# Kernel tuning notes

Measured on AMD Instinct MI355X. Metric: run time of the kernel, lower is better.

## Reference

```python
import jax, jax.numpy as jnp
import numpy as np

B, A, C, M, E = 8, 100000, 8, 128, 32
ALPHA, GAMMA = 0.25, 2.0


def setup_inputs() -> dict:
    key = jax.random.key(0)
    k1, k2, k3, k4, k5, k6, k7 = jax.random.split(key, 7)
    classifications = jax.random.uniform(k1, (B, A, C), dtype=jnp.float32)
    regressions = jax.random.normal(k2, (B, A, 8), dtype=jnp.float32)
    embeddings = jax.random.normal(k3, (B, A, E), dtype=jnp.float32)
    # anchors: random centers on a 1920x1080 image, reasonable w/h -> x1,y1,x2,y2
    cx = jax.random.uniform(k4, (A,), minval=0.0, maxval=1920.0)
    cy = jax.random.uniform(jax.random.fold_in(k4, 1), (A,), minval=0.0, maxval=1080.0)
    w = jax.random.uniform(jax.random.fold_in(k4, 2), (A,), minval=16.0, maxval=256.0)
    h = jax.random.uniform(jax.random.fold_in(k4, 3), (A,), minval=16.0, maxval=256.0)
    anchors = jnp.stack([cx - 0.5 * w, cy - 0.5 * h, cx + 0.5 * w, cy + 0.5 * h], axis=1)[None].astype(jnp.float32)
    # annotations: 16 coords = jittered 3D-box corner projections around a random box,
    # col 16 = object id, col 17 = class label in [0, C)
    bcx = jax.random.uniform(k5, (B, M, 1), minval=100.0, maxval=1820.0)
    bcy = jax.random.uniform(jax.random.fold_in(k5, 1), (B, M, 1), minval=100.0, maxval=980.0)
    bw = jax.random.uniform(jax.random.fold_in(k5, 2), (B, M, 1), minval=30.0, maxval=300.0)
    bh = jax.random.uniform(jax.random.fold_in(k5, 3), (B, M, 1), minval=30.0, maxval=300.0)
    jit = jax.random.uniform(k6, (B, M, 16), minval=-0.4, maxval=0.4)
    sx = jnp.array([-1, -1, 1, 1, -1, -1, 1, 1], jnp.float32)
    sy = jnp.array([-1, 1, -1, 1, -1, 1, -1, 1], jnp.float32)
    xs = bcx + 0.5 * bw * (sx + jit[..., 0:16:2])
    ys = bcy + 0.5 * bh * (sy + jit[..., 1:16:2])
    coords = jnp.stack([xs, ys], axis=-1).reshape(B, M, 16)
    ids = jax.random.randint(k7, (B, M, 1), 0, 1000).astype(jnp.float32)
    cls_lab = jax.random.randint(jax.random.fold_in(k7, 1), (B, M, 1), 0, C).astype(jnp.float32)
    annotations = jnp.concatenate([coords, ids, cls_lab], axis=-1)
    return {
        "classifications": classifications,
        "regressions": regressions,
        "anchors": anchors,
        "annotations": annotations,
        "embeddings": embeddings,
    }


def calc_iou(a, b):
    # a: [A,4], b: [M,4] in x1,y1,x2,y2 -> [A,M]
    area = (b[:, 2] - b[:, 0]) * (b[:, 3] - b[:, 1])
    iw = jnp.minimum(a[:, 2:3], b[None, :, 2]) - jnp.maximum(a[:, 0:1], b[None, :, 0])
    ih = jnp.minimum(a[:, 3:4], b[None, :, 3]) - jnp.maximum(a[:, 1:2], b[None, :, 1])
    iw = jnp.clip(iw, 0.0)
    ih = jnp.clip(ih, 0.0)
    ua = ((a[:, 2] - a[:, 0]) * (a[:, 3] - a[:, 1]))[:, None] + area[None, :] - iw * ih
    return iw * ih / jnp.clip(ua, 1e-8)


_S2 = jnp.array([-1, -1, 1, 1, -1, -1, 1, 1], jnp.float32)
_S4 = jnp.array([-1, 1, -1, 1, -1, 1, -1, 1], jnp.float32)
_S6 = jnp.array([1, 1, 1, 1, -1, -1, -1, -1], jnp.float32)


def _per_image(cls, reg, ann, anchor):
    # cls [A,C], reg [A,8], ann [M,18], anchor [A,4]
    aw = anchor[:, 2] - anchor[:, 0]
    ah = anchor[:, 3] - anchor[:, 1]
    acx = anchor[:, 0] + 0.5 * aw
    acy = anchor[:, 1] + 0.5 * ah
    cls = jnp.clip(cls, 1e-4, 1.0 - 1e-4)
    valid = ann[:, -1] >= 0.0  # [M]; annotations with class -1 are padding
    xs, ys = ann[:, 0:16:2], ann[:, 1:16:2]
    box2d = jnp.stack([xs.min(1), ys.min(1), xs.max(1), ys.max(1)], axis=1)  # [M,4]
    iou = jnp.where(valid[None, :], calc_iou(anchor, box2d), -1.0)  # [A,M]
    iou_max = iou.max(1)
    assigned = ann[iou.argmax(1)]  # [A,18]
    pos = iou_max >= 0.5
    neg = iou_max < 0.4
    num_pos = jnp.maximum(pos.sum().astype(cls.dtype), 1.0)

    onehot = jax.nn.one_hot(assigned[:, -1].astype(jnp.int32), cls.shape[1], dtype=cls.dtype)
    targets = jnp.where(pos[:, None], onehot, jnp.where(neg[:, None], 0.0, -1.0))
    alpha_f = jnp.where(targets == 1.0, ALPHA, 1.0 - ALPHA)
    focal_w = alpha_f * jnp.where(targets == 1.0, 1.0 - cls, cls) ** GAMMA
    bce = -(targets * jnp.log(cls) + (1.0 - targets) * jnp.log(1.0 - cls))
    cls_loss = jnp.where(targets != -1.0, focal_w * bce, 0.0).sum() / num_pos

    t = assigned[:, :16]

    def vp(rx, ry, tx, ty):
        denom = jnp.sqrt(rx * rx + ry * ry) * jnp.sqrt(tx * tx + ty * ty)
        return 1.0 - (rx * tx + ry * ty) / jnp.maximum(denom, 1e-8)

    vp1 = vp(reg[:, 2], reg[:, 3],
             (t[:, 4] + t[:, 6] + t[:, 12] + t[:, 14] - (t[:, 0] + t[:, 2] + t[:, 8] + t[:, 10])) / 4.0,
             (t[:, 5] + t[:, 7] + t[:, 13] + t[:, 15] - (t[:, 1] + t[:, 3] + t[:, 9] + t[:, 11])) / 4.0)
    vp2 = vp(reg[:, 4], reg[:, 5],
             (t[:, 2] + t[:, 6] + t[:, 10] + t[:, 14] - (t[:, 0] + t[:, 4] + t[:, 8] + t[:, 12])) / 4.0,
             (t[:, 3] + t[:, 7] + t[:, 11] + t[:, 15] - (t[:, 1] + t[:, 5] + t[:, 9] + t[:, 13])) / 4.0)
    vp3 = vp(reg[:, 6], reg[:, 7],
             (t[:, 0] + t[:, 2] + t[:, 4] + t[:, 6] - (t[:, 8] + t[:, 10] + t[:, 12] + t[:, 14])) / 4.0,
             (t[:, 1] + t[:, 3] + t[:, 5] + t[:, 7] - (t[:, 9] + t[:, 11] + t[:, 13] + t[:, 15])) / 4.0)
    vp_all = (vp1 + vp2 + vp3) / 3.0
    vp_loss = (vp_all * pos).sum() / num_pos

    # corner predictions from (ctr_x, ctr_y, v1, v2, v3) offsets: [A,8] x-coords, [A,8] y-coords
    px = reg[:, 0:1] + reg[:, 2:3] * _S2 + reg[:, 4:5] * _S4 + reg[:, 6:7] * _S6
    py = reg[:, 1:2] + reg[:, 3:4] * _S2 + reg[:, 5:6] * _S4 + reg[:, 7:8] * _S6
    tx = (t[:, 0:16:2] - acx[:, None]) / aw[:, None]
    ty = (t[:, 1:16:2] - acy[:, None]) / ah[:, None]
    diff = jnp.concatenate([jnp.abs(px - tx), jnp.abs(py - ty)], axis=1)  # [A,16]
    sl1 = jnp.where(diff <= 1.0 / 9.0, 0.5 * 9.0 * diff * diff, diff - 0.5 / 9.0)
    reg_loss = (sl1.mean(1) * pos).sum() / num_pos
    return cls_loss, reg_loss, vp_loss


def reference(classifications, regressions, anchors, annotations, embeddings):
    anchor = anchors[0]
    cls_l, reg_l, vp_l = jax.vmap(_per_image, in_axes=(0, 0, 0, None))(
        classifications, regressions, annotations, anchor)
    return jnp.stack([cls_l.mean(), reg_l.mean(), vp_l.mean()])


if __name__ == "__main__":
    print(reference(**setup_inputs()))
```

## Files before the change

kernel.cpp:

```cpp
#include <hip/hip_runtime.h>

namespace {

constexpr int B_N = 8;
constexpr int A_N = 100000;
constexpr int M_N = 128;
constexpr int BLOCK = 256;
constexpr int NBLK_S = (A_N + BLOCK - 1) / BLOCK;
constexpr int GX = 16, GY = 9, NC = GX * GY;
constexpr float CELL = 120.0f;
constexpr float MARGIN = 128.0f;
constexpr int CPC = 4;
constexpr int NCH = NC * CPC;

constexpr size_t OFF_HIST = 0;
constexpr size_t OFF_OFFS = OFF_HIST + (size_t)NBLK_S * NC * 4;
constexpr size_t OFF_CT   = OFF_OFFS + (size_t)NC * NBLK_S * 4;
constexpr size_t OFF_CB   = OFF_CT + NC * 4;
constexpr size_t OFF_SIDX = (OFF_CB + (NC + 1) * 4 + 15) & ~size_t(15);
constexpr size_t OFF_SANC = (OFF_SIDX + (size_t)A_N * 4 + 15) & ~size_t(15);
constexpr size_t OFF_SNEG = OFF_SANC + (size_t)A_N * 16;
constexpr size_t OFF_PART = OFF_SNEG + (size_t)B_N * A_N * 4;

__device__ __forceinline__ int cell_of(const float4& an) {
    const float acx = 0.5f * (an.x + an.z);
    const float acy = 0.5f * (an.y + an.w);
    const int cx = min(GX - 1, max(0, (int)(acx * (1.0f / CELL))));
    const int cy = min(GY - 1, max(0, (int)(acy * (1.0f / CELL))));
    return cy * GX + cx;
}

__global__ __launch_bounds__(BLOCK) void s1k(
    const float* __restrict__ anchors_,
    const float* __restrict__ cls_,
    unsigned* __restrict__ hist,
    float* __restrict__ sneg_)
{
    __shared__ unsigned h[NC];
    const int tid = threadIdx.x, blk = blockIdx.x;
    for (int i = tid; i < NC; i += BLOCK) h[i] = 0u;
    __syncthreads();
    const int a = blk * BLOCK + tid;
    if (a < A_N) {
        const float4 an = ((const float4*)anchors_)[a];
        atomicAdd(&h[cell_of(an)], 1u);
#pragma unroll
        for (int b = 0; b < B_N; ++b) {
            const float* cp = cls_ + ((size_t)b * A_N + a) * 8;
            const float4 cA = ((const float4*)cp)[0];
            const float4 cB = ((const float4*)cp)[1];
            const float pv[8] = {cA.x, cA.y, cA.z, cA.w, cB.x, cB.y, cB.z, cB.w};
            float s = 0.f;
#pragma unroll
            for (int c = 0; c < 8; ++c) {
                const float p = fminf(fmaxf(pv[c], 1e-4f), 1.0f - 1e-4f);
                s += 0.75f * p * p * (-__logf(1.0f - p));
            }
            sneg_[(size_t)b * A_N + a] = s;
        }
    }
    __syncthreads();
    for (int i = tid; i < NC; i += BLOCK) hist[(size_t)blk * NC + i] = h[i];
}

__global__ __launch_bounds__(BLOCK) void s2a_scan(
    const unsigned* __restrict__ hist,
    unsigned* __restrict__ offs,
    unsigned* __restrict__ cellTot)
{
    const int c = blockIdx.x, t = threadIdx.x;
    const int k0 = 2 * t, k1 = 2 * t + 1;
    const unsigned v0 = (k0 < NBLK_S) ? hist[(size_t)k0 * NC + c] : 0u;
    const unsigned v1 = (k1 < NBLK_S) ? hist[(size_t)k1 * NC + c] : 0u;
    const unsigned mysum = v0 + v1;
    __shared__ unsigned s[BLOCK];
    s[t] = mysum;
    __syncthreads();
    for (int off = 1; off < BLOCK; off <<= 1) {
        const unsigned x = (t >= off) ? s[t - off] : 0u;
        __syncthreads();
        s[t] += x;
        __syncthreads();
    }
    const unsigned excl = s[t] - mysum;
    if (k0 < NBLK_S) offs[(size_t)c * NBLK_S + k0] = excl;
    if (k1 < NBLK_S) offs[(size_t)c * NBLK_S + k1] = excl + v0;
    if (t == BLOCK - 1) cellTot[c] = s[BLOCK - 1];
}

__global__ __launch_bounds__(BLOCK) void s3_scatter(
    const float* __restrict__ anchors_,
    const unsigned* __restrict__ offs,
    const unsigned* __restrict__ cellTot,
    unsigned* __restrict__ cellBase,
    unsigned* __restrict__ sidx, float4* __restrict__ sanc)
{
    __shared__ unsigned sscan[BLOCK];
    __shared__ unsigned scb[NC];
    __shared__ unsigned hw[4][NC];
    const int tid = threadIdx.x, blk = blockIdx.x;

    const unsigned v = (tid < NC) ? cellTot[tid] : 0u;
    sscan[tid] = v;
    for (int i = tid; i < 4 * NC; i += BLOCK) (&hw[0][0])[i] = 0u;
    __syncthreads();
    for (int off = 1; off < BLOCK; off <<= 1) {
        const unsigned x = (tid >= off) ? sscan[tid - off] : 0u;
        __syncthreads();
        sscan[tid] += x;
        __syncthreads();
    }
    if (tid < NC) scb[tid] = sscan[tid] - v;
    if (blk == 0) {
        if (tid < NC) cellBase[tid] = sscan[tid] - v;
        if (tid == NC - 1) cellBase[NC] = sscan[tid];
    }

    const int a = blk * BLOCK + tid;
    const bool valid = (a < A_N);
    float4 an = make_float4(0.f, 0.f, 0.f, 0.f);
    int c = -1;
    if (valid) { an = ((const float4*)anchors_)[a]; c = cell_of(an); }
    const int ln = tid & 63, wv = tid >> 6;

    int rank = 0, cnt = 0;
    for (int j = 0; j < 64; ++j) {
        const int cj = __shfl(c, j);
        const bool same = (cj == c);
        rank += (same && (j < ln));
        cnt  += same;
    }
    if (valid && rank == 0) hw[wv][c] = (unsigned)cnt;
    __syncthreads();
    if (valid) {
        unsigned r = (unsigned)rank;
        for (int w = 0; w < wv; ++w) r += hw[w][c];
        const unsigned d = scb[c] + offs[(size_t)c * NBLK_S + blk] + r;
        sidx[d] = (unsigned)a;
        sanc[d] = an;
    }
}

__global__ __launch_bounds__(BLOCK) void ka2(
    const float* __restrict__ cls_,
    const float* __restrict__ reg_,
    const float* __restrict__ ann_,
    const float* __restrict__ sneg_,
    const unsigned* __restrict__ cellBase,
    const unsigned* __restrict__ sidx,
    const float4* __restrict__ sanc,
    float* __restrict__ partials)
{
    const int cc = blockIdx.x / CPC, chunk = blockIdx.x % CPC;
    const int b = blockIdx.y, tid = threadIdx.x;
    const int base = (int)cellBase[cc];
    const int n    = (int)cellBase[cc + 1] - base;

    if (chunk * BLOCK >= n) {
        if (tid == 0) {
            float* o = partials + ((size_t)b * NCH + blockIdx.x) * 4;
            o[0] = 0.f; o[1] = 0.f; o[2] = 0.f; o[3] = 0.f;
        }
        return;
    }

    __shared__ float s_x1[M_N], s_y1[M_N], s_x2[M_N], s_y2[M_N], s_nb[M_N];
    __shared__ int   s_id[M_N];
    __shared__ unsigned long long s_w[2];
    __shared__ unsigned s_pre[2];
    __shared__ int s_Kv;

    const int ccx = cc % GX, ccy = cc / GX;
    const float lox = ccx * CELL - MARGIN, hix = ccx * CELL + CELL + MARGIN;
    const float loy = ccy * CELL - MARGIN, hiy = ccy * CELL + CELL + MARGIN;
    bool ok = false;
    float minx = 0.f, miny = 0.f, maxx = 0.f, maxy = 0.f, area = 0.f;
    if (tid < M_N) {
        const float* t = ann_ + ((size_t)b * M_N + tid) * 18;
        minx = t[0]; maxx = t[0]; miny = t[1]; maxy = t[1];
#pragma unroll
        for (int j = 1; j < 8; ++j) {
            const float x = t[2 * j], y = t[2 * j + 1];
            minx = fminf(minx, x); maxx = fmaxf(maxx, x);
            miny = fminf(miny, y); maxy = fmaxf(maxy, y);
        }
        area = (maxx - minx) * (maxy - miny);
        ok = (t[17] >= 0.0f) && (minx <= hix) && (maxx >= lox) &&
             (miny <= hiy) && (maxy >= loy);
    }
    const unsigned long long bw = __ballot(ok);
    if (tid < 128 && (tid & 63) == 0) s_w[tid >> 6] = bw;
    __syncthreads();
    if (tid == 0) {
        const unsigned p0 = (unsigned)__popcll(s_w[0]);
        s_pre[0] = 0u; s_pre[1] = p0;
        s_Kv = (int)(p0 + (unsigned)__popcll(s_w[1]));
    }
    __syncthreads();
    if (ok) {
        const int wq = tid >> 6;
        const int r = (int)(s_pre[wq] +
            (unsigned)__popcll(s_w[wq] & ((1ull << (tid & 63)) - 1ull)));
        s_x1[r] = minx; s_y1[r] = miny;
        s_x2[r] = maxx; s_y2[r] = maxy;
        s_nb[r] = -area;
        s_id[r] = tid;
    }
    __syncthreads();
    const int K = s_Kv;

    const int i0  = chunk * BLOCK + tid;
    const bool inb = (i0 < n);
    const int gi  = base + (inb ? i0 : 0);
    const float4 an = sanc[gi];
    const int a = (int)sidx[gi];
    const float sneg_v = sneg_[(size_t)b * A_N + a];

    const float aarea = (an.z - an.x) * (an.w - an.y);
    float m1 = -3e38f, m2 = -3e38f;
    float bn = 0.f, bs = 1.f;
    int   kb = 0;

    for (int m = 0; m < K; ++m) {
        const float x1 = s_x1[m], y1 = s_y1[m];
        const float x2 = s_x2[m], y2 = s_y2[m];
        const float nb = s_nb[m];
        const float iw = fminf(an.z, x2) - fmaxf(an.x, x1);
        const float ih = fminf(an.w, y2) - fmaxf(an.y, y1);
        const float in_ = fmaxf(iw, 0.f) * fmaxf(ih, 0.f);
        m1 = fmaxf(m1, __builtin_fmaf(3.0f, in_, nb));
        m2 = fmaxf(m2, __builtin_fmaf(3.5f, in_, nb));
        const float s = aarea - nb;
        const bool  u = (in_ * bs > bn * s);
        bn = u ? in_ : bn;
        bs = u ? s   : bs;
        kb = u ? m   : kb;
    }

    const bool pos = inb && (m1 >= aarea);
    const bool nonign = pos || (m2 < aarea);

    float clsS = (inb && nonign) ? sneg_v : 0.f;
    float regS = 0.f, vpS = 0.f, posC = 0.f;

    if (pos) {
        posC = 1.0f;
        const float* t = ann_ + ((size_t)b * M_N + s_id[kb]) * 18;
        float tt[16];
#pragma unroll
        for (int j = 0; j < 16; ++j) tt[j] = t[j];
        const int kc = (int)t[17];

        const float praw = cls_[((size_t)b * A_N + a) * 8 + kc];
        const float pkc = fminf(fmaxf(praw, 1e-4f), 1.0f - 1e-4f);
        const float negkc   = 0.75f * pkc * pkc * (-__logf(1.0f - pkc));
        const float posterm = 0.25f * (1.0f - pkc) * (1.0f - pkc) * (-__logf(pkc));
        clsS += posterm - negkc;

        const float aw = an.z - an.x;
        const float ah = an.w - an.y;
        const float* rp = reg_ + ((size_t)b * A_N + a) * 8;
        const float4 r0 = ((const float4*)rp)[0];
        const float4 r1 = ((const float4*)rp)[1];

        auto vp = [](float rx, float ry, float tx, float ty) {
            const float denom = sqrtf(rx * rx + ry * ry) * sqrtf(tx * tx + ty * ty);
            return 1.0f - (rx * tx + ry * ty) / fmaxf(denom, 1e-8f);
        };
        const float vp1 = vp(r0.z, r0.w,
            (tt[4] + tt[6] + tt[12] + tt[14] - (tt[0] + tt[2] + tt[8] + tt[10])) * 0.25f,
            (tt[5] + tt[7] + tt[13] + tt[15] - (tt[1] + tt[3] + tt[9] + tt[11])) * 0.25f);
        const float vp2 = vp(r1.x, r1.y,
            (tt[2] + tt[6] + tt[10] + tt[14] - (tt[0] + tt[4] + tt[8] + tt[12])) * 0.25f,
            (tt[3] + tt[7] + tt[11] + tt[15] - (tt[1] + tt[5] + tt[9] + tt[13])) * 0.25f);
        const float vp3 = vp(r1.z, r1.w,
            (tt[0] + tt[2] + tt[4] + tt[6] - (tt[8] + tt[10] + tt[12] + tt[14])) * 0.25f,
            (tt[1] + tt[3] + tt[5] + tt[7] - (tt[9] + tt[11] + tt[13] + tt[15])) * 0.25f);
        vpS = (vp1 + vp2 + vp3) * (1.0f / 3.0f);

        const float s2v[8] = {-1, -1, 1, 1, -1, -1, 1, 1};
        const float s4v[8] = {-1, 1, -1, 1, -1, 1, -1, 1};
        const float s6v[8] = {1, 1, 1, 1, -1, -1, -1, -1};
        const float acx2 = an.x + 0.5f * aw;
        const float acy2 = an.y + 0.5f * ah;
        float ssum = 0.f;
#pragma unroll
        for (int j = 0; j < 8; ++j) {
            const float px = r0.x + r0.z * s2v[j] + r1.x * s4v[j] + r1.z * s6v[j];
            const float py = r0.y + r0.w * s2v[j] + r1.y * s4v[j] + r1.w * s6v[j];
            const float tx = (tt[2 * j]     - acx2) / aw;
            const float ty = (tt[2 * j + 1] - acy2) / ah;
            const float dx = fabsf(px - tx);
            const float dy = fabsf(py - ty);
            ssum += (dx <= (1.0f / 9.0f)) ? 4.5f * dx * dx : dx - (0.5f / 9.0f);
            ssum += (dy <= (1.0f / 9.0f)) ? 4.5f * dy * dy : dy - (0.5f / 9.0f);
        }
        regS = ssum * (1.0f / 16.0f);
    }

#pragma unroll
    for (int off = 32; off; off >>= 1) {
        clsS += __shfl_down(clsS, off);
        regS += __shfl_down(regS, off);
        vpS  += __shfl_down(vpS, off);
        posC += __shfl_down(posC, off);
    }
    __shared__ float s_red[4][4];
    const int wv = tid >> 6, ln = tid & 63;
    if (ln == 0) {
        s_red[wv][0] = clsS; s_red[wv][1] = regS;
        s_red[wv][2] = vpS;  s_red[wv][3] = posC;
    }
    __syncthreads();
    if (tid == 0) {
        float C = 0, R = 0, V = 0, P = 0;
        for (int w2 = 0; w2 < 4; ++w2) {
            C += s_red[w2][0]; R += s_red[w2][1];
            V += s_red[w2][2]; P += s_red[w2][3];
        }
        float* out = partials + ((size_t)b * NCH + blockIdx.x) * 4;
        out[0] = C; out[1] = R; out[2] = V; out[3] = P;
    }
}

__global__ __launch_bounds__(BLOCK) void kc_final(
    const float* __restrict__ partials,
    float* __restrict__ out)
{
    const int tid = threadIdx.x;
    __shared__ float s[4][4];
    __shared__ float accum[3];
    if (tid == 0) { accum[0] = 0.f; accum[1] = 0.f; accum[2] = 0.f; }

    for (int b = 0; b < B_N; ++b) {
        float c = 0.f, r = 0.f, v = 0.f, p = 0.f;
        for (int i = tid; i < NCH; i += BLOCK) {
            const float* q = partials + ((size_t)b * NCH + i) * 4;
            c += q[0]; r += q[1]; v += q[2]; p += q[3];
        }
#pragma unroll
        for (int off = 32; off; off >>= 1) {
            c += __shfl_down(c, off); r += __shfl_down(r, off);
            v += __shfl_down(v, off); p += __shfl_down(p, off);
        }
        const int wv = tid >> 6, ln = tid & 63;
        if (ln == 0) { s[wv][0] = c; s[wv][1] = r; s[wv][2] = v; s[wv][3] = p; }
        __syncthreads();
        if (tid == 0) {
            float C = 0, R = 0, V = 0, P = 0;
            for (int w = 0; w < 4; ++w) {
                C += s[w][0]; R += s[w][1]; V += s[w][2]; P += s[w][3];
            }
            const float np_ = fmaxf(P, 1.0f);
            accum[0] += C / np_; accum[1] += R / np_; accum[2] += V / np_;
        }
        __syncthreads();
    }
    if (tid == 0) {
        out[0] = accum[0] * 0.125f;
        out[1] = accum[1] * 0.125f;
        out[2] = accum[2] * 0.125f;
    }
}

}

extern "C" void kernel_launch(void* const* d_in, const int* in_sizes, int n_in,
                              void* d_out, int out_size, void* d_ws, size_t ws_size,
                              hipStream_t stream)
{
    const float* cls_    = (const float*)d_in[0];
    const float* reg_    = (const float*)d_in[1];
    const float* anchors = (const float*)d_in[2];
    const float* ann     = (const float*)d_in[3];

    char* ws = (char*)d_ws;
    unsigned* hist     = (unsigned*)(ws + OFF_HIST);
    unsigned* offs     = (unsigned*)(ws + OFF_OFFS);
    unsigned* cellTot  = (unsigned*)(ws + OFF_CT);
    unsigned* cellBase = (unsigned*)(ws + OFF_CB);
    unsigned* sidxp    = (unsigned*)(ws + OFF_SIDX);
    float4*   sancp    = (float4*)(ws + OFF_SANC);
    float*    snegp    = (float*)(ws + OFF_SNEG);
    float*    partials = (float*)(ws + OFF_PART);

    s1k<<<dim3(NBLK_S), dim3(BLOCK), 0, stream>>>(anchors, cls_, hist, snegp);
    s2a_scan<<<dim3(NC), dim3(BLOCK), 0, stream>>>(hist, offs, cellTot);
    s3_scatter<<<dim3(NBLK_S), dim3(BLOCK), 0, stream>>>(anchors, offs, cellTot,
                                                         cellBase, sidxp, sancp);
    ka2<<<dim3(NCH, B_N), dim3(BLOCK), 0, stream>>>(
        cls_, reg_, ann, snegp, cellBase, sidxp, sancp, partials);
    kc_final<<<dim3(1), dim3(BLOCK), 0, stream>>>(partials, (float*)d_out);
}
```

Before: 63.51 us.

## Precompute per-cell box lists and loop batches inside the IoU kernel

Building the per-(batch, cell) filtered annotation lists moves out of the IoU kernel and into the first kernel, which gets extra blocks to write them to a workspace buffer along with counts. The IoU kernel now launches one block per cell chunk instead of one per (chunk, batch). Each block loops over all eight batches, reusing its anchor and index loads and copying the prebuilt box records into shared memory. This removes redundant annotation filtering and anchor reloads, but cuts the grid size eightfold and serializes batch work within a block, which may reduce latency hiding.

```diff
diff --git a/kernel.cpp b/kernel.cpp
--- a/kernel.cpp
+++ b/kernel.cpp
@@ -20,7 +20,9 @@
 constexpr size_t OFF_SIDX = (OFF_CB + (NC + 1) * 4 + 15) & ~size_t(15);
 constexpr size_t OFF_SANC = (OFF_SIDX + (size_t)A_N * 4 + 15) & ~size_t(15);
 constexpr size_t OFF_SNEG = OFF_SANC + (size_t)A_N * 16;
-constexpr size_t OFF_PART = OFF_SNEG + (size_t)B_N * A_N * 4;
+constexpr size_t OFF_BL   = OFF_SNEG + (size_t)B_N * A_N * 4;
+constexpr size_t OFF_KL   = OFF_BL + (size_t)B_N * NC * M_N * 8 * 4;
+constexpr size_t OFF_PART = (OFF_KL + (size_t)B_N * NC * 4 + 15) & ~size_t(15);
 
 __device__ __forceinline__ int cell_of(const float4& an) {
     const float acx = 0.5f * (an.x + an.z);
@@ -30,37 +32,81 @@
     return cy * GX + cx;
 }
 
-__global__ __launch_bounds__(BLOCK) void s1k(
+__global__ __launch_bounds__(BLOCK) void s1kx(
     const float* __restrict__ anchors_,
     const float* __restrict__ cls_,
+    const float* __restrict__ ann_,
     unsigned* __restrict__ hist,
-    float* __restrict__ sneg_)
+    float* __restrict__ sneg_,
+    float* __restrict__ bl,
+    unsigned* __restrict__ kl)
 {
     __shared__ unsigned h[NC];
-    const int tid = threadIdx.x, blk = blockIdx.x;
-    for (int i = tid; i < NC; i += BLOCK) h[i] = 0u;
+    __shared__ unsigned long long s_w[2];
+    __shared__ unsigned s_pre[2];
+    const int blk = blockIdx.x, tid = threadIdx.x;
+
+    if (blk < NBLK_S) {
+        for (int i = tid; i < NC; i += BLOCK) h[i] = 0u;
+        __syncthreads();
+        const int a = blk * BLOCK + tid;
+        if (a < A_N) {
+            const float4 an = ((const float4*)anchors_)[a];
+            atomicAdd(&h[cell_of(an)], 1u);
+#pragma unroll
+            for (int b = 0; b < B_N; ++b) {
+                const float* cp = cls_ + ((size_t)b * A_N + a) * 8;
+                const float4 cA = ((const float4*)cp)[0];
+                const float4 cB = ((const float4*)cp)[1];
+                const float pv[8] = {cA.x, cA.y, cA.z, cA.w, cB.x, cB.y, cB.z, cB.w};
+                float s = 0.f;
+#pragma unroll
+                for (int c = 0; c < 8; ++c) {
+                    const float p = fminf(fmaxf(pv[c], 1e-4f), 1.0f - 1e-4f);
+                    s += 0.75f * p * p * (-__logf(1.0f - p));
+                }
+                sneg_[(size_t)b * A_N + a] = s;
+            }
+        }
+        __syncthreads();
+        for (int i = tid; i < NC; i += BLOCK) hist[(size_t)blk * NC + i] = h[i];
+        return;
+    }
+
+    const int bi = blk - NBLK_S;
+    const int b  = bi / NC, cc = bi % NC;
+    const int ccx = cc % GX, ccy = cc / GX;
+    const float lox = ccx * CELL - MARGIN, hix = ccx * CELL + CELL + MARGIN;
+    const float loy = ccy * CELL - MARGIN, hiy = ccy * CELL + CELL + MARGIN;
+    bool ok = false;
+    float minx = 0.f, miny = 0.f, maxx = 0.f, maxy = 0.f, area = 0.f;
+    if (tid < M_N) {
+        const float* t = ann_ + ((size_t)b * M_N + tid) * 18;
+        minx = t[0]; maxx = t[0]; miny = t[1]; maxy = t[1];
+#pragma unroll
+        for (int j = 1; j < 8; ++j) {
+            const float x = t[2 * j], y = t[2 * j + 1];
+            minx = fminf(minx, x); maxx = fmaxf(maxx, x);
+            miny = fminf(miny, y); maxy = fmaxf(maxy, y);
+        }
+        area = (maxx - minx) * (maxy - miny);
+        ok = (t[17] >= 0.0f) && (minx <= hix) && (maxx >= lox) &&
+             (miny <= hiy) && (maxy >= loy);
+    }
+    const unsigned long long bw = __ballot(ok);
+    if (tid < 128 && (tid & 63) == 0) s_w[tid >> 6] = bw;
     __syncthreads();
-    const int a = blk * BLOCK + tid;
-    if (a < A_N) {
-        const float4 an = ((const float4*)anchors_)[a];
-        atomicAdd(&h[cell_of(an)], 1u);
-#pragma unroll
-        for (int b = 0; b < B_N; ++b) {
-            const float* cp = cls_ + ((size_t)b * A_N + a) * 8;
-            const float4 cA = ((const float4*)cp)[0];
-            const float4 cB = ((const float4*)cp)[1];
-            const float pv[8] = {cA.x, cA.y, cA.z, cA.w, cB.x, cB.y, cB.z, cB.w};
-            float s = 0.f;
-#pragma unroll
-            for (int c = 0; c < 8; ++c) {
-                const float p = fminf(fmaxf(pv[c], 1e-4f), 1.0f - 1e-4f);
-                s += 0.75f * p * p * (-__logf(1.0f - p));
-            }
-            sneg_[(size_t)b * A_N + a] = s;
-        }
-    }
-    __syncthreads();
-    for (int i = tid; i < NC; i += BLOCK) hist[(size_t)blk * NC + i] = h[i];
+    const unsigned p0 = (unsigned)__popcll(s_w[0]);
+    if (ok) {
+        const int wq = tid >> 6;
+        const int r = (int)((wq ? p0 : 0u) +
+            (unsigned)__popcll(s_w[wq] & ((1ull << (tid & 63)) - 1ull)));
+        float* o = bl + (((size_t)b * NC + cc) * M_N + r) * 8;
+        o[0] = minx; o[1] = miny; o[2] = maxx; o[3] = maxy;
+        o[4] = -area; o[5] = (float)tid; o[6] = 0.f; o[7] = 0.f;
+    }
+    if (tid == 0)
+        kl[(size_t)b * NC + cc] = p0 + (unsigned)__popcll(s_w[1]);
 }
 
 __global__ __launch_bounds__(BLOCK) void s2a_scan(
@@ -141,7 +187,7 @@
     }
 }
 
-__global__ __launch_bounds__(BLOCK) void ka2(
+__global__ __launch_bounds__(BLOCK) void ka3(
     const float* __restrict__ cls_,
     const float* __restrict__ reg_,
     const float* __restrict__ ann_,
@@ -149,177 +195,145 @@
     const unsigned* __restrict__ cellBase,
     const unsigned* __restrict__ sidx,
     const float4* __restrict__ sanc,
+    const float* __restrict__ bl,
+    const unsigned* __restrict__ kl,
     float* __restrict__ partials)
 {
     const int cc = blockIdx.x / CPC, chunk = blockIdx.x % CPC;
-    const int b = blockIdx.y, tid = threadIdx.x;
+    const int tid = threadIdx.x;
     const int base = (int)cellBase[cc];
     const int n    = (int)cellBase[cc + 1] - base;
 
     if (chunk * BLOCK >= n) {
-        if (tid == 0) {
-            float* o = partials + ((size_t)b * NCH + blockIdx.x) * 4;
-            o[0] = 0.f; o[1] = 0.f; o[2] = 0.f; o[3] = 0.f;
+        if (tid < B_N * 4) {
+            partials[((size_t)(tid >> 2) * NCH + blockIdx.x) * 4 + (tid & 3)] = 0.f;
         }
         return;
     }
 
-    __shared__ float s_x1[M_N], s_y1[M_N], s_x2[M_N], s_y2[M_N], s_nb[M_N];
-    __shared__ int   s_id[M_N];
-    __shared__ unsigned long long s_w[2];
-    __shared__ unsigned s_pre[2];
-    __shared__ int s_Kv;
-
-    const int ccx = cc % GX, ccy = cc / GX;
-    const float lox = ccx * CELL - MARGIN, hix = ccx * CELL + CELL + MARGIN;
-    const float loy = ccy * CELL - MARGIN, hiy = ccy * CELL + CELL + MARGIN;
-    bool ok = false;
-    float minx = 0.f, miny = 0.f, maxx = 0.f, maxy = 0.f, area = 0.f;
-    if (tid < M_N) {
-        const float* t = ann_ + ((size_t)b * M_N + tid) * 18;
-        minx = t[0]; maxx = t[0]; miny = t[1]; maxy = t[1];
-#pragma unroll
-        for (int j = 1; j < 8; ++j) {
-            const float x = t[2 * j], y = t[2 * j + 1];
-            minx = fminf(minx, x); maxx = fmaxf(maxx, x);
-            miny = fminf(miny, y); maxy = fmaxf(maxy, y);
-        }
-        area = (maxx - minx) * (maxy - miny);
-        ok = (t[17] >= 0.0f) && (minx <= hix) && (maxx >= lox) &&
-             (miny <= hiy) && (maxy >= loy);
-    }
-    const unsigned long long bw = __ballot(ok);
-    if (tid < 128 && (tid & 63) == 0) s_w[tid >> 6] = bw;
-    __syncthreads();
-    if (tid == 0) {
-        const unsigned p0 = (unsigned)__popcll(s_w[0]);
-        s_pre[0] = 0u; s_pre[1] = p0;
-        s_Kv = (int)(p0 + (unsigned)__popcll(s_w[1]));
-    }
-    __syncthreads();
-    if (ok) {
-        const int wq = tid >> 6;
-        const int r = (int)(s_pre[wq] +
-            (unsigned)__popcll(s_w[wq] & ((1ull << (tid & 63)) - 1ull)));
-        s_x1[r] = minx; s_y1[r] = miny;
-        s_x2[r] = maxx; s_y2[r] = maxy;
-        s_nb[r] = -area;
-        s_id[r] = tid;
-    }
-    __syncthreads();
-    const int K = s_Kv;
+    __shared__ float s_rec[M_N][8];
+    __shared__ float s_red[4][4];
 
     const int i0  = chunk * BLOCK + tid;
     const bool inb = (i0 < n);
     const int gi  = base + (inb ? i0 : 0);
     const float4 an = sanc[gi];
     const int a = (int)sidx[gi];
-    const float sneg_v = sneg_[(size_t)b * A_N + a];
-
     const float aarea = (an.z - an.x) * (an.w - an.y);
-    float m1 = -3e38f, m2 = -3e38f;
-    float bn = 0.f, bs = 1.f;
-    int   kb = 0;
-
-    for (int m = 0; m < K; ++m) {
-        const float x1 = s_x1[m], y1 = s_y1[m];
-        const float x2 = s_x2[m], y2 = s_y2[m];
-        const float nb = s_nb[m];
-        const float iw = fminf(an.z, x2) - fmaxf(an.x, x1);
-        const float ih = fminf(an.w, y2) - fmaxf(an.y, y1);
-        const float in_ = fmaxf(iw, 0.f) * fmaxf(ih, 0.f);
-        m1 = fmaxf(m1, __builtin_fmaf(3.0f, in_, nb));
-        m2 = fmaxf(m2, __builtin_fmaf(3.5f, in_, nb));
-        const float s = aarea - nb;
-        const bool  u = (in_ * bs > bn * s);
-        bn = u ? in_ : bn;
-        bs = u ? s   : bs;
-        kb = u ? m   : kb;
-    }
-
-    const bool pos = inb && (m1 >= aarea);
-    const bool nonign = pos || (m2 < aarea);
-
-    float clsS = (inb && nonign) ? sneg_v : 0.f;
-    float regS = 0.f, vpS = 0.f, posC = 0.f;
-
-    if (pos) {
-        posC = 1.0f;
-        const float* t = ann_ + ((size_t)b * M_N + s_id[kb]) * 18;
-        float tt[16];
-#pragma unroll
-        for (int j = 0; j < 16; ++j) tt[j] = t[j];
-        const int kc = (int)t[17];
-
-        const float praw = cls_[((size_t)b * A_N + a) * 8 + kc];
-        const float pkc = fminf(fmaxf(praw, 1e-4f), 1.0f - 1e-4f);
-        const float negkc   = 0.75f * pkc * pkc * (-__logf(1.0f - pkc));
-        const float posterm = 0.25f * (1.0f - pkc) * (1.0f - pkc) * (-__logf(pkc));
-        clsS += posterm - negkc;
-
-        const float aw = an.z - an.x;
-        const float ah = an.w - an.y;
-        const float* rp = reg_ + ((size_t)b * A_N + a) * 8;
-        const float4 r0 = ((const float4*)rp)[0];
-        const float4 r1 = ((const float4*)rp)[1];
-
-        auto vp = [](float rx, float ry, float tx, float ty) {
-            const float denom = sqrtf(rx * rx + ry * ry) * sqrtf(tx * tx + ty * ty);
-            return 1.0f - (rx * tx + ry * ty) / fmaxf(denom, 1e-8f);
-        };
-        const float vp1 = vp(r0.z, r0.w,
-            (tt[4] + tt[6] + tt[12] + tt[14] - (tt[0] + tt[2] + tt[8] + tt[10])) * 0.25f,
-            (tt[5] + tt[7] + tt[13] + tt[15] - (tt[1] + tt[3] + tt[9] + tt[11])) * 0.25f);
-        const float vp2 = vp(r1.x, r1.y,
-            (tt[2] + tt[6] + tt[10] + tt[14] - (tt[0] + tt[4] + tt[8] + tt[12])) * 0.25f,
-            (tt[3] + tt[7] + tt[11] + tt[15] - (tt[1] + tt[5] + tt[9] + tt[13])) * 0.25f);
-        const float vp3 = vp(r1.z, r1.w,
-            (tt[0] + tt[2] + tt[4] + tt[6] - (tt[8] + tt[10] + tt[12] + tt[14])) * 0.25f,
-            (tt[1] + tt[3] + tt[5] + tt[7] - (tt[9] + tt[11] + tt[13] + tt[15])) * 0.25f);
-        vpS = (vp1 + vp2 + vp3) * (1.0f / 3.0f);
-
-        const float s2v[8] = {-1, -1, 1, 1, -1, -1, 1, 1};
-        const float s4v[8] = {-1, 1, -1, 1, -1, 1, -1, 1};
-        const float s6v[8] = {1, 1, 1, 1, -1, -1, -1, -1};
-        const float acx2 = an.x + 0.5f * aw;
-        const float acy2 = an.y + 0.5f * ah;
-        float ssum = 0.f;
-#pragma unroll
-        for (int j = 0; j < 8; ++j) {
-            const float px = r0.x + r0.z * s2v[j] + r1.x * s4v[j] + r1.z * s6v[j];
-            const float py = r0.y + r0.w * s2v[j] + r1.y * s4v[j] + r1.w * s6v[j];
-            const float tx = (tt[2 * j]     - acx2) / aw;
-            const float ty = (tt[2 * j + 1] - acy2) / ah;
-            const float dx = fabsf(px - tx);
-            const float dy = fabsf(py - ty);
-            ssum += (dx <= (1.0f / 9.0f)) ? 4.5f * dx * dx : dx - (0.5f / 9.0f);
-            ssum += (dy <= (1.0f / 9.0f)) ? 4.5f * dy * dy : dy - (0.5f / 9.0f);
-        }
-        regS = ssum * (1.0f / 16.0f);
-    }
-
-#pragma unroll
-    for (int off = 32; off; off >>= 1) {
-        clsS += __shfl_down(clsS, off);
-        regS += __shfl_down(regS, off);
-        vpS  += __shfl_down(vpS, off);
-        posC += __shfl_down(posC, off);
-    }
-    __shared__ float s_red[4][4];
     const int wv = tid >> 6, ln = tid & 63;
-    if (ln == 0) {
-        s_red[wv][0] = clsS; s_red[wv][1] = regS;
-        s_red[wv][2] = vpS;  s_red[wv][3] = posC;
-    }
-    __syncthreads();
-    if (tid == 0) {
-        float C = 0, R = 0, V = 0, P = 0;
-        for (int w2 = 0; w2 < 4; ++w2) {
-            C += s_red[w2][0]; R += s_red[w2][1];
-            V += s_red[w2][2]; P += s_red[w2][3];
-        }
-        float* out = partials + ((size_t)b * NCH + blockIdx.x) * 4;
-        out[0] = C; out[1] = R; out[2] = V; out[3] = P;
+
+    for (int b = 0; b < B_N; ++b) {
+        const int K = (int)kl[(size_t)b * NC + cc];
+        const float sneg_v = inb ? sneg_[(size_t)b * A_N + a] : 0.f;
+        if (tid < K) {
+            const float4* src = (const float4*)(bl + (((size_t)b * NC + cc) * M_N + tid) * 8);
+            ((float4*)s_rec[tid])[0] = src[0];
+            ((float4*)s_rec[tid])[1] = src[1];
+        }
+        __syncthreads();
+
+        float m1 = -3e38f, m2 = -3e38f;
+        float bn = 0.f, bs = 1.f;
+        int   kb = 0;
+        for (int m = 0; m < K; ++m) {
+            const float x1 = s_rec[m][0], y1 = s_rec[m][1];
+            const float x2 = s_rec[m][2], y2 = s_rec[m][3];
+            const float nb = s_rec[m][4];
+            const float iw = fminf(an.z, x2) - fmaxf(an.x, x1);
+            const float ih = fminf(an.w, y2) - fmaxf(an.y, y1);
+            const float in_ = fmaxf(iw, 0.f) * fmaxf(ih, 0.f);
+            m1 = fmaxf(m1, __builtin_fmaf(3.0f, in_, nb));
+            m2 = fmaxf(m2, __builtin_fmaf(3.5f, in_, nb));
+            const float s = aarea - nb;
+            const bool  u = (in_ * bs > bn * s);
+            bn = u ? in_ : bn;
+            bs = u ? s   : bs;
+            kb = u ? m   : kb;
+        }
+
+        const bool pos = inb && (m1 >= aarea);
+        const bool nonign = pos || (m2 < aarea);
+
+        float clsS = (inb && nonign) ? sneg_v : 0.f;
+        float regS = 0.f, vpS = 0.f, posC = 0.f;
+
+        if (pos) {
+            posC = 1.0f;
+            const int bid = (int)s_rec[kb][5];
+            const float* t = ann_ + ((size_t)b * M_N + bid) * 18;
+            float tt[16];
+#pragma unroll
+            for (int j = 0; j < 16; ++j) tt[j] = t[j];
+            const int kc = (int)t[17];
+
+            const float praw = cls_[((size_t)b * A_N + a) * 8 + kc];
+            const float pkc = fminf(fmaxf(praw, 1e-4f), 1.0f - 1e-4f);
+            const float negkc   = 0.75f * pkc * pkc * (-__logf(1.0f - pkc));
+            const float posterm = 0.25f * (1.0f - pkc) * (1.0f - pkc) * (-__logf(pkc));
+            clsS += posterm - negkc;
+
+            const float aw = an.z - an.x;
+            const float ah = an.w - an.y;
+            const float* rp = reg_ + ((size_t)b * A_N + a) * 8;
+            const float4 r0 = ((const float4*)rp)[0];
+            const float4 r1 = ((const float4*)rp)[1];
+
+            auto vp = [](float rx, float ry, float tx, float ty) {
+                const float denom = sqrtf(rx * rx + ry * ry) * sqrtf(tx * tx + ty * ty);
+                return 1.0f - (rx * tx + ry * ty) / fmaxf(denom, 1e-8f);
+            };
+            const float vp1 = vp(r0.z, r0.w,
+                (tt[4] + tt[6] + tt[12] + tt[14] - (tt[0] + tt[2] + tt[8] + tt[10])) * 0.25f,
+                (tt[5] + tt[7] + tt[13] + tt[15] - (tt[1] + tt[3] + tt[9] + tt[11])) * 0.25f);
+            const float vp2 = vp(r1.x, r1.y,
+                (tt[2] + tt[6] + tt[10] + tt[14] - (tt[0] + tt[4] + tt[8] + tt[12])) * 0.25f,
+                (tt[3] + tt[7] + tt[11] + tt[15] - (tt[1] + tt[5] + tt[9] + tt[13])) * 0.25f);
+            const float vp3 = vp(r1.z, r1.w,
+                (tt[0] + tt[2] + tt[4] + tt[6] - (tt[8] + tt[10] + tt[12] + tt[14])) * 0.25f,
+                (tt[1] + tt[3] + tt[5] + tt[7] - (tt[9] + tt[11] + tt[13] + tt[15])) * 0.25f);
+            vpS = (vp1 + vp2 + vp3) * (1.0f / 3.0f);
+
+            const float s2v[8] = {-1, -1, 1, 1, -1, -1, 1, 1};
+            const float s4v[8] = {-1, 1, -1, 1, -1, 1, -1, 1};
+            const float s6v[8] = {1, 1, 1, 1, -1, -1, -1, -1};
+            const float acx2 = an.x + 0.5f * aw;
+            const float acy2 = an.y + 0.5f * ah;
+            float ssum = 0.f;
+#pragma unroll
+            for (int j = 0; j < 8; ++j) {
+                const float px = r0.x + r0.z * s2v[j] + r1.x * s4v[j] + r1.z * s6v[j];
+                const float py = r0.y + r0.w * s2v[j] + r1.y * s4v[j] + r1.w * s6v[j];
+                const float tx = (tt[2 * j]     - acx2) / aw;
+                const float ty = (tt[2 * j + 1] - acy2) / ah;
+                const float dx = fabsf(px - tx);
+                const float dy = fabsf(py - ty);
+                ssum += (dx <= (1.0f / 9.0f)) ? 4.5f * dx * dx : dx - (0.5f / 9.0f);
+                ssum += (dy <= (1.0f / 9.0f)) ? 4.5f * dy * dy : dy - (0.5f / 9.0f);
+            }
+            regS = ssum * (1.0f / 16.0f);
+        }
+
+#pragma unroll
+        for (int off = 32; off; off >>= 1) {
+            clsS += __shfl_down(clsS, off);
+            regS += __shfl_down(regS, off);
+            vpS  += __shfl_down(vpS, off);
+            posC += __shfl_down(posC, off);
+        }
+        if (ln == 0) {
+            s_red[wv][0] = clsS; s_red[wv][1] = regS;
+            s_red[wv][2] = vpS;  s_red[wv][3] = posC;
+        }
+        __syncthreads();
+        if (tid == 0) {
+            float C = 0, R = 0, V = 0, P = 0;
+            for (int w2 = 0; w2 < 4; ++w2) {
+                C += s_red[w2][0]; R += s_red[w2][1];
+                V += s_red[w2][2]; P += s_red[w2][3];
+            }
+            float* out = partials + ((size_t)b * NCH + blockIdx.x) * 4;
+            out[0] = C; out[1] = R; out[2] = V; out[3] = P;
+        }
     }
 }
 
@@ -382,13 +396,16 @@
     unsigned* sidxp    = (unsigned*)(ws + OFF_SIDX);
     float4*   sancp    = (float4*)(ws + OFF_SANC);
     float*    snegp    = (float*)(ws + OFF_SNEG);
+    float*    blp      = (float*)(ws + OFF_BL);
+    unsigned* klp      = (unsigned*)(ws + OFF_KL);
     float*    partials = (float*)(ws + OFF_PART);
 
-    s1k<<<dim3(NBLK_S), dim3(BLOCK), 0, stream>>>(anchors, cls_, hist, snegp);
+    s1kx<<<dim3(NBLK_S + B_N * NC), dim3(BLOCK), 0, stream>>>(
+        anchors, cls_, ann, hist, snegp, blp, klp);
     s2a_scan<<<dim3(NC), dim3(BLOCK), 0, stream>>>(hist, offs, cellTot);
     s3_scatter<<<dim3(NBLK_S), dim3(BLOCK), 0, stream>>>(anchors, offs, cellTot,
                                                          cellBase, sidxp, sancp);
-    ka2<<<dim3(NCH, B_N), dim3(BLOCK), 0, stream>>>(
-        cls_, reg_, ann, snegp, cellBase, sidxp, sancp, partials);
+    ka3<<<dim3(NCH), dim3(BLOCK), 0, stream>>>(
+        cls_, reg_, ann, snegp, cellBase, sidxp, sancp, blp, klp, partials);
     kc_final<<<dim3(1), dim3(BLOCK), 0, stream>>>(partials, (float*)d_out);
 }
```

Result: slower. 79.96 us (+25.9%).
